# Performance work log

Measured on AMD Instinct MI355X. Metric: run time of the kernel, lower is better.

Reference implementation:

```python
import jax, jax.numpy as jnp
import numpy as np

THRESHOLD = 6.0  # bnb MatmulLtState outlier threshold


def setup_inputs() -> dict:
    key = jax.random.key(0)
    k1, k2, k3, k4, k5 = jax.random.split(key, 5)
    B, S, DIN, DOUT = 4, 2048, 4096, 16384
    x = jax.random.normal(k1, (B, S, DIN), dtype=jnp.float32).astype(jnp.float16)
    # inject a few outlier feature columns (|x| > threshold) so the LLM.int8()
    # mixed-precision decomposition path is actually exercised
    out_cols = jax.random.randint(k5, (8,), 0, DIN)
    x = x.at[:, :, out_cols].multiply(10.0)
    # CB: int8 codebook values stored as fp16 (bnb keeps them as int8; math is identical)
    CB = jnp.round(jax.random.uniform(k2, (DOUT, DIN), minval=-127.0, maxval=127.0)).astype(jnp.float16)
    SCB = jax.random.uniform(k3, (DOUT, 1), minval=0.5, maxval=2.0).astype(jnp.float16)
    bias = (jax.random.normal(k4, (DOUT,)) * 0.01).astype(jnp.float16)
    return {"x": x, "CB": CB, "SCB": SCB, "bias": bias}


def _llm_int8_matmul(x, CB, SCB, bias, threshold):
    # forward: weight = CB * SCB / 127 (dequantized fp16 weight), then bnb's
    # mixed int8 matmul with outlier-column decomposition (has_fp16_weights=True)
    W = CB.astype(jnp.float32) * SCB.astype(jnp.float32) / 127.0  # [DOUT, DIN]
    xf = x.astype(jnp.float32)
    lead = xf.shape[:-1]
    X = xf.reshape(-1, xf.shape[-1])  # [N, DIN]

    # outlier columns: any row has |x| > threshold in that feature column
    col_out = (jnp.abs(X) > threshold).any(axis=0)  # [DIN] bool
    X_out = jnp.where(col_out[None, :], X, 0.0)      # fp16-path activations
    X_in = jnp.where(col_out[None, :], 0.0, X)       # int8-path activations

    # per-row (per-token) absmax int8 quantization of inlier activations
    sx = jnp.maximum(jnp.max(jnp.abs(X_in), axis=1, keepdims=True), 1e-8)  # [N,1]
    Xq = jnp.clip(jnp.round(X_in * (127.0 / sx)), -127.0, 127.0)

    # per-output-row absmax int8 quantization of the (dequantized) weight
    sw = jnp.maximum(jnp.max(jnp.abs(W), axis=1, keepdims=True), 1e-8)  # [DOUT,1]
    Wq = jnp.clip(jnp.round(W * (127.0 / sw)), -127.0, 127.0)

    # int8 GEMM (emulated in fp32) + dequant with outer product of scales
    out = (Xq @ Wq.T) * (sx * sw.T) * (1.0 / (127.0 * 127.0))  # [N, DOUT]
    # fp16 outlier path: only the outlier weight columns participate
    out = out + X_out @ jnp.where(col_out[None, :], W, 0.0).T
    out = out + bias.astype(jnp.float32)[None, :]
    return out.reshape(*lead, W.shape[0]).astype(jnp.float16)


def reference(x, CB, SCB, bias):
    return _llm_int8_matmul(x, CB, SCB, bias, THRESHOLD)
```

## Files before the change

kernel.cpp:

```cpp
#include <hip/hip_runtime.h>
#include <hip/hip_fp16.h>
#include <stdint.h>

typedef int v4i __attribute__((ext_vector_type(4)));

__device__ __forceinline__ void gld_lds16(const void* g, void* l) {
    __builtin_amdgcn_global_load_lds(
        (const __attribute__((address_space(1))) void*)g,
        (__attribute__((address_space(3))) void*)l,
        16, 0, 0);
}

#define ENDBAR() do { __builtin_amdgcn_s_barrier(); __builtin_amdgcn_sched_barrier(0); } while (0)
#define VMC(n)   asm volatile("s_waitcnt vmcnt(" #n ")" ::: "memory")
#define VMLG0()  asm volatile("s_waitcnt vmcnt(0) lgkmcnt(0)" ::: "memory")

__global__ __launch_bounds__(256) void k_flags(const float* __restrict__ x,
                                               unsigned int* __restrict__ flags,
                                               int total4, int DIN) {
    int idx = blockIdx.x * blockDim.x + threadIdx.x;
    int stride = gridDim.x * blockDim.x;
    int dmask = DIN - 1;
    for (int i = idx; i < total4; i += stride) {
        float4 v = ((const float4*)x)[i];
        int base = i * 4;
        if (fabsf(v.x) > 6.0f) atomicOr(&flags[(base + 0) & dmask], 1u);
        if (fabsf(v.y) > 6.0f) atomicOr(&flags[(base + 1) & dmask], 1u);
        if (fabsf(v.z) > 6.0f) atomicOr(&flags[(base + 2) & dmask], 1u);
        if (fabsf(v.w) > 6.0f) atomicOr(&flags[(base + 3) & dmask], 1u);
    }
}

__global__ __launch_bounds__(256) void k_build(const unsigned int* __restrict__ flags,
                                               unsigned char* __restrict__ bmask,
                                               int* __restrict__ ncols,
                                               int* __restrict__ cols, int DIN) {
    __shared__ int wcnt[4];
    __shared__ int base;
    int tid = threadIdx.x, lane = tid & 63, wid = tid >> 6;
    if (tid == 0) base = 0;
    __syncthreads();
    for (int c0 = 0; c0 < DIN; c0 += 256) {
        int c = c0 + tid;
        bool p = (c < DIN) && (flags[c] != 0u);
        if (c < DIN) bmask[c] = p ? 1 : 0;
        unsigned long long m = __ballot(p);
        int wpre = __popcll(m & ((1ull << lane) - 1ull));
        if (lane == 0) wcnt[wid] = __popcll(m);
        __syncthreads();
        int pre = 0;
        for (int w = 0; w < wid; w++) pre += wcnt[w];
        if (p) cols[base + pre + wpre] = c;
        __syncthreads();
        if (tid == 0) base += wcnt[0] + wcnt[1] + wcnt[2] + wcnt[3];
        __syncthreads();
    }
    if (tid == 0) *ncols = base;
}

__global__ __launch_bounds__(256) void k_quantx(const float* __restrict__ x,
                                                const unsigned char* __restrict__ bmask,
                                                signed char* __restrict__ Xq,
                                                float* __restrict__ sx, int DIN) {
    int row = blockIdx.x;
    int tid = threadIdx.x, lane = tid & 63, wid = tid >> 6;
    const float* xr = x + (size_t)row * DIN;
    float f[16];
    #pragma unroll
    for (int j = 0; j < 4; j++) {
        float4 v = ((const float4*)xr)[tid * 4 + j];
        f[4*j] = v.x; f[4*j+1] = v.y; f[4*j+2] = v.z; f[4*j+3] = v.w;
    }
    uint4 bm4 = ((const uint4*)bmask)[tid];
    const unsigned char* bm = (const unsigned char*)&bm4;
    float m = 0.0f;
    #pragma unroll
    for (int j = 0; j < 16; j++) {
        if (bm[j]) f[j] = 0.0f;
        m = fmaxf(m, fabsf(f[j]));
    }
    #pragma unroll
    for (int off = 32; off >= 1; off >>= 1) m = fmaxf(m, __shfl_xor(m, off));
    __shared__ float red[4];
    if (lane == 0) red[wid] = m;
    __syncthreads();
    m = fmaxf(fmaxf(red[0], red[1]), fmaxf(red[2], red[3]));
    float sxv = fmaxf(m, 1e-8f);
    if (Xq) {
        float scale = 127.0f / sxv;
        int qi[16];
        #pragma unroll
        for (int j = 0; j < 16; j++) {
            float r = rintf(f[j] * scale);
            r = fminf(127.0f, fmaxf(-127.0f, r));
            qi[j] = (int)r;
        }
        int4 ov;
        ov.x = (qi[0]&0xff) | ((qi[1]&0xff)<<8) | ((qi[2]&0xff)<<16) | ((qi[3]&0xff)<<24);
        ov.y = (qi[4]&0xff) | ((qi[5]&0xff)<<8) | ((qi[6]&0xff)<<16) | ((qi[7]&0xff)<<24);
        ov.z = (qi[8]&0xff) | ((qi[9]&0xff)<<8) | ((qi[10]&0xff)<<16) | ((qi[11]&0xff)<<24);
        ov.w = (qi[12]&0xff) | ((qi[13]&0xff)<<8) | ((qi[14]&0xff)<<16) | ((qi[15]&0xff)<<24);
        ((int4*)(Xq + (size_t)row * DIN))[tid] = ov;
    }
    if (tid == 0) sx[row] = sxv;
}

__global__ __launch_bounds__(256) void k_quantw(const float* __restrict__ CB,
                                                const float* __restrict__ SCB,
                                                signed char* __restrict__ Wq,
                                                float* __restrict__ sw, int DIN) {
    int row = blockIdx.x;
    int tid = threadIdx.x, lane = tid & 63, wid = tid >> 6;
    float scb = SCB[row];
    const float* cr = CB + (size_t)row * DIN;
    float w[16];
    #pragma unroll
    for (int j = 0; j < 4; j++) {
        float4 v = ((const float4*)cr)[tid * 4 + j];
        w[4*j]   = v.x * scb / 127.0f;
        w[4*j+1] = v.y * scb / 127.0f;
        w[4*j+2] = v.z * scb / 127.0f;
        w[4*j+3] = v.w * scb / 127.0f;
    }
    float m = 0.0f;
    #pragma unroll
    for (int j = 0; j < 16; j++) m = fmaxf(m, fabsf(w[j]));
    #pragma unroll
    for (int off = 32; off >= 1; off >>= 1) m = fmaxf(m, __shfl_xor(m, off));
    __shared__ float red[4];
    if (lane == 0) red[wid] = m;
    __syncthreads();
    m = fmaxf(fmaxf(red[0], red[1]), fmaxf(red[2], red[3]));
    float swv = fmaxf(m, 1e-8f);
    if (Wq) {
        float scale = 127.0f / swv;
        int qi[16];
        #pragma unroll
        for (int j = 0; j < 16; j++) {
            float r = rintf(w[j] * scale);
            r = fminf(127.0f, fmaxf(-127.0f, r));
            qi[j] = (int)r;
        }
        int4 ov;
        ov.x = (qi[0]&0xff) | ((qi[1]&0xff)<<8) | ((qi[2]&0xff)<<16) | ((qi[3]&0xff)<<24);
        ov.y = (qi[4]&0xff) | ((qi[5]&0xff)<<8) | ((qi[6]&0xff)<<16) | ((qi[7]&0xff)<<24);
        ov.z = (qi[8]&0xff) | ((qi[9]&0xff)<<8) | ((qi[10]&0xff)<<16) | ((qi[11]&0xff)<<24);
        ov.w = (qi[12]&0xff) | ((qi[13]&0xff)<<8) | ((qi[14]&0xff)<<16) | ((qi[15]&0xff)<<24);
        ((int4*)(Wq + (size_t)row * DIN))[tid] = ov;
    }
    if (tid == 0) sw[row] = swv;
}

__global__ __launch_bounds__(256) void k_outpanels(
    const float* __restrict__ x, const float* __restrict__ CB,
    const float* __restrict__ SCB, const int* __restrict__ ncols,
    const int* __restrict__ cols, float* __restrict__ Xout, float* __restrict__ Wout,
    int Nrows, int DOUT, int DIN)
{
    int nc = *ncols;
    int ncl = nc < 16 ? nc : 16;
    int idx = blockIdx.x * 256 + threadIdx.x;
    int row = idx >> 4, c = idx & 15;
    if (row >= Nrows + DOUT) return;
    float v = 0.0f;
    if (row < Nrows) {
        if (c < ncl) v = x[(size_t)row * DIN + cols[c]];
        Xout[row * 16 + c] = v;
    } else {
        int j = row - Nrows;
        if (c < ncl) v = CB[(size_t)j * DIN + cols[c]] * SCB[j] / 127.0f;
        Wout[j * 16 + c] = v;
    }
}

__global__ __launch_bounds__(512) void k_gemm8(
    const signed char* __restrict__ Xq, const signed char* __restrict__ Wq,
    const float* __restrict__ sx, const float* __restrict__ sw,
    const float* __restrict__ x, const float* __restrict__ CB,
    const float* __restrict__ SCB, const float* __restrict__ bias,
    const float* __restrict__ Xout, const float* __restrict__ Wout,
    const int* __restrict__ ncols, const int* __restrict__ cols,
    float* __restrict__ out, int Nrows, int DOUT, int DIN)
{
    __shared__ __align__(16) char LDS[131072];

    const int tid = threadIdx.x, lane = tid & 63, wid = tid >> 6;
    const int wm = wid >> 2, wn = wid & 3;

    int nwg = gridDim.x, bid = blockIdx.x;
    int swzb;
    if ((nwg & 7) == 0) { int cpx = nwg >> 3; swzb = (bid & 7) * cpx + (bid >> 3); }
    else swzb = bid;
    int mtiles = Nrows >> 8;
    int ntiles = DOUT >> 8;
    int mt, ntl;
    if ((mtiles & 7) == 0 && (ntiles & 3) == 0 && (nwg & 31) == 0) {
        int group = swzb >> 5, local = swzb & 31;
        int mrects = mtiles >> 3;
        int mt_r = group % mrects, nt_r = group / mrects;
        mt  = (mt_r << 3) + (local & 7);
        ntl = (nt_r << 2) + (local >> 3);
    } else {
        mt = swzb % mtiles; ntl = swzb / mtiles;
    }
    int brow = mt << 8, bcol = ntl << 8;

    const int o0 = 16 * ((lane >> 4) ^ ((lane >> 1) & 7));
    const int o1 = o0 ^ 64;
    const int aRow = (wm * 128 + (lane & 15)) * 128;
    const int bRow = (wn * 64 + (lane & 15)) * 128;

    const int stRow = wid * 8 + (lane >> 3);
    const int stCol = 16 * ((lane & 7) ^ (((wid & 1) << 2) + (lane >> 4)));
    const signed char* aSrc = Xq + (size_t)(brow + stRow) * DIN + stCol;
    const signed char* bSrc = Wq + (size_t)(bcol + stRow) * DIN + stCol;
    const int ldsW = wid * 1024;

    v4i acc[8][4] = {};
    v4i a0[8], a1[8], b0[4], b1[4];

    const int nt = DIN >> 7;
    const int NIT = nt >> 1;

#define STAGE_HALF(srcBase, matOff, bf, h, kc)                                   \
    do { _Pragma("unroll")                                                        \
      for (int q = 0; q < 2; q++) {                                               \
        int seg = 2*(h) + q;                                                      \
        gld_lds16((srcBase) + (size_t)seg * 64 * DIN + (kc),                      \
                  &LDS[(matOff) + (bf)*32768 + seg*8192 + ldsW]);                 \
      }                                                                           \
    } while (0)

#define DS_A(dst, bf, miB)                                                        \
    do { _Pragma("unroll")                                                        \
      for (int mi = 0; mi < 4; mi++) {                                            \
        int ro = (bf)*32768 + aRow + ((miB) + mi) * 2048;                         \
        dst[mi*2+0] = *(const v4i*)&LDS[ro + o0];                                 \
        dst[mi*2+1] = *(const v4i*)&LDS[ro + o1];                                 \
      }                                                                           \
    } while (0)

#define DS_B(dst, bf, niB)                                                        \
    do { _Pragma("unroll")                                                        \
      for (int ni = 0; ni < 2; ni++) {                                            \
        int ro = 65536 + (bf)*32768 + bRow + ((niB) + ni) * 2048;                 \
        dst[ni*2+0] = *(const v4i*)&LDS[ro + o0];                                 \
        dst[ni*2+1] = *(const v4i*)&LDS[ro + o1];                                 \
      }                                                                           \
    } while (0)

#define QUAD(A8, B4, accM, accN)                                                  \
    do { __builtin_amdgcn_s_setprio(1); _Pragma("unroll")                         \
      for (int mi = 0; mi < 4; mi++) { _Pragma("unroll")                          \
        for (int ni = 0; ni < 2; ni++) { _Pragma("unroll")                        \
          for (int ks = 0; ks < 2; ks++)                                          \
            acc[(accM)+mi][(accN)+ni] = __builtin_amdgcn_mfma_i32_16x16x64_i8(    \
                A8[mi*2+ks], B4[ni*2+ks], acc[(accM)+mi][(accN)+ni], 0, 0, 0);    \
        } }                                                                       \
      __builtin_amdgcn_s_setprio(0);                                              \
    } while (0)

    STAGE_HALF(aSrc, 0,     0, 0, 0);
    STAGE_HALF(aSrc, 0,     0, 1, 0);
    STAGE_HALF(bSrc, 65536, 0, 0, 0);
    STAGE_HALF(bSrc, 65536, 0, 1, 0);
    STAGE_HALF(aSrc, 0,     1, 0, 128);
    STAGE_HALF(aSrc, 0,     1, 1, 128);
    VMC(4);
    ENDBAR();

    for (int it = 0; it < NIT; ++it) {
        int t = 2 * it;
        int kB1 = (t + 1) << 7;
        int tA2 = t + 2; if (tA2 > nt - 1) tA2 = nt - 1;
        int kA2 = tA2 << 7;
        int tA3 = t + 3; if (tA3 > nt - 1) tA3 = nt - 1;
        int kA3 = tA3 << 7;

        STAGE_HALF(bSrc, 65536, 1, 0, kB1);
        DS_B(b0, 0, 0); DS_A(a0, 0, 0);
        QUAD(a0, b0, 0, 0);
        STAGE_HALF(bSrc, 65536, 1, 1, kB1);
        DS_A(a1, 0, 4);
        QUAD(a1, b0, 4, 0);
        ENDBAR();
        STAGE_HALF(aSrc, 0, 0, 0, kA2);
        DS_B(b1, 0, 2);
        QUAD(a1, b1, 4, 2);
        STAGE_HALF(aSrc, 0, 0, 1, kA2);
        QUAD(a0, b1, 0, 2);
        VMC(4);
        ENDBAR();
        STAGE_HALF(bSrc, 65536, 0, 0, kA2);
        DS_B(b0, 1, 0); DS_A(a0, 1, 0);
        QUAD(a0, b0, 0, 0);
        STAGE_HALF(bSrc, 65536, 0, 1, kA2);
        DS_A(a1, 1, 4);
        QUAD(a1, b0, 4, 0);
        ENDBAR();
        STAGE_HALF(aSrc, 0, 1, 0, kA3);
        DS_B(b1, 1, 2);
        QUAD(a1, b1, 4, 2);
        STAGE_HALF(aSrc, 0, 1, 1, kA3);
        QUAD(a0, b1, 0, 2);
        VMC(4);
        ENDBAR();
    }
    VMLG0();
    ENDBAR();

    int nc = *ncols;
    int ncl = nc < 16 ? nc : 16;
    float* Xo = (float*)&LDS[0];
    float* Wo = (float*)&LDS[65536];
    for (int idx = tid; idx < 4096; idx += 512) {
        int i = idx >> 4, c = idx & 15;
        Xo[i * 17 + c] = Xout[(size_t)(brow + i) * 16 + c];
        Wo[i * 17 + c] = Wout[(size_t)(bcol + i) * 16 + c];
    }
    __syncthreads();

    float sww[4], bzz[4];
    #pragma unroll
    for (int ni = 0; ni < 4; ni++) {
        int gcol = bcol + wn * 64 + ni * 16 + (lane & 15);
        sww[ni] = sw[gcol];
        bzz[ni] = bias[gcol];
    }

    #pragma unroll
    for (int h = 0; h < 2; h++) {
        float vout[4][4][4];
        #pragma unroll
        for (int mi = 0; mi < 4; mi++) {
            int row = wm * 128 + (h * 4 + mi) * 16 + (lane >> 4) * 4;
            #pragma unroll
            for (int r = 0; r < 4; r++) {
                float sxv = sx[brow + row + r];
                #pragma unroll
                for (int ni = 0; ni < 4; ni++)
                    vout[mi][ni][r] =
                        ((float)acc[h * 4 + mi][ni][r] * (sxv * sww[ni])) * (1.0f / 16129.0f);
            }
        }
        for (int c = 0; c < ncl; c++) {
            float wo[4];
            #pragma unroll
            for (int ni = 0; ni < 4; ni++)
                wo[ni] = Wo[(wn * 64 + ni * 16 + (lane & 15)) * 17 + c];
            #pragma unroll
            for (int mi = 0; mi < 4; mi++) {
                int row = wm * 128 + (h * 4 + mi) * 16 + (lane >> 4) * 4;
                #pragma unroll
                for (int r = 0; r < 4; r++) {
                    float xo = Xo[(row + r) * 17 + c];
                    #pragma unroll
                    for (int ni = 0; ni < 4; ni++)
                        vout[mi][ni][r] += xo * wo[ni];
                }
            }
        }
        #pragma unroll
        for (int mi = 0; mi < 4; mi++) {
            #pragma unroll
            for (int ni = 0; ni < 4; ni++) {
                int gcol = bcol + wn * 64 + ni * 16 + (lane & 15);
                #pragma unroll
                for (int r = 0; r < 4; r++) {
                    int grow = brow + wm * 128 + (h * 4 + mi) * 16 + (lane >> 4) * 4 + r;
                    float v = vout[mi][ni][r];
                    for (int c = 16; c < nc; c++) {
                        int col = cols[c];
                        v += x[(size_t)grow * DIN + col] *
                             (CB[(size_t)gcol * DIN + col] * SCB[gcol] / 127.0f);
                    }
                    v += bzz[ni];
                    v = __half2float(__float2half(v));
                    out[(size_t)grow * DOUT + gcol] = v;
                }
            }
        }
    }
#undef STAGE_HALF
#undef DS_A
#undef DS_B
#undef QUAD
}

template<int FLY>
__global__ __launch_bounds__(256) void k_gemm(
    const signed char* __restrict__ Xq, const signed char* __restrict__ Wq,
    const float* __restrict__ sx, const float* __restrict__ sw,
    const float* __restrict__ x, const float* __restrict__ CB,
    const float* __restrict__ SCB, const float* __restrict__ bias,
    const unsigned char* __restrict__ bmask,
    const int* __restrict__ ncols, const int* __restrict__ cols,
    float* __restrict__ out, int Nrows, int DOUT, int DIN)
{
    __shared__ __align__(16) signed char Asm[128 * 64];
    __shared__ __align__(16) signed char Bsm[128 * 64];

    int nwg = gridDim.x;
    int bid = blockIdx.x;
    int swzb;
    if ((nwg & 7) == 0) { int cpx = nwg >> 3; swzb = (bid & 7) * cpx + (bid >> 3); }
    else swzb = bid;
    int mtiles = Nrows >> 7;
    int mt = swzb % mtiles;
    int nt = swzb / mtiles;
    int brow = mt << 7, bcol = nt << 7;

    int tid = threadIdx.x, lane = tid & 63, wid = tid >> 6;
    int wr = wid >> 1, wc = wid & 1;

    v4i acc[4][4] = {};

    int arow = wr * 64 + (lane & 15);
    int brl  = wc * 64 + (lane & 15);
    int kc   = (lane >> 4) * 16;

    if constexpr (FLY == 0) {
        int srow = lane >> 2;
        int scol = (lane & 3) * 16;
        const signed char* ga0 = Xq + (size_t)(brow + wid * 16 + srow) * DIN + scol;
        const signed char* ga1 = Xq + (size_t)(brow + (wid + 4) * 16 + srow) * DIN + scol;
        const signed char* gb0 = Wq + (size_t)(bcol + wid * 16 + srow) * DIN + scol;
        const signed char* gb1 = Wq + (size_t)(bcol + (wid + 4) * 16 + srow) * DIN + scol;
        signed char* la0 = &Asm[wid * 1024];
        signed char* la1 = &Asm[(wid + 4) * 1024];
        signed char* lb0 = &Bsm[wid * 1024];
        signed char* lb1 = &Bsm[(wid + 4) * 1024];

        for (int k0 = 0; k0 < DIN; k0 += 64) {
            gld_lds16(ga0 + k0, la0);
            gld_lds16(ga1 + k0, la1);
            gld_lds16(gb0 + k0, lb0);
            gld_lds16(gb1 + k0, lb1);
            __syncthreads();
            v4i a[4], b[4];
            #pragma unroll
            for (int mi = 0; mi < 4; mi++) a[mi] = *(const v4i*)&Asm[(arow + mi * 16) * 64 + kc];
            #pragma unroll
            for (int ni = 0; ni < 4; ni++) b[ni] = *(const v4i*)&Bsm[(brl + ni * 16) * 64 + kc];
            #pragma unroll
            for (int mi = 0; mi < 4; mi++)
                #pragma unroll
                for (int ni = 0; ni < 4; ni++)
                    acc[mi][ni] = __builtin_amdgcn_mfma_i32_16x16x64_i8(a[mi], b[ni], acc[mi][ni], 0, 0, 0);
            __syncthreads();
        }
    } else {
        int ra = tid >> 1, ca = (tid & 1) * 32;
        const float* xrow = x  + (size_t)(brow + ra) * DIN + ca;
        const float* crow = CB + (size_t)(bcol + ra) * DIN + ca;
        float xscale = 127.0f / sx[brow + ra];
        float scb    = SCB[bcol + ra];
        float wscale = 127.0f / sw[bcol + ra];
        signed char* lda = &Asm[ra * 64 + ca];
        signed char* ldb = &Bsm[ra * 64 + ca];

        for (int k0 = 0; k0 < DIN; k0 += 64) {
            float xa[32], wb[32];
            #pragma unroll
            for (int j = 0; j < 8; j++) {
                float4 v = ((const float4*)(xrow + k0))[j];
                xa[4*j] = v.x; xa[4*j+1] = v.y; xa[4*j+2] = v.z; xa[4*j+3] = v.w;
                float4 u = ((const float4*)(crow + k0))[j];
                wb[4*j] = u.x; wb[4*j+1] = u.y; wb[4*j+2] = u.z; wb[4*j+3] = u.w;
            }
            uint4 bm0 = *(const uint4*)(bmask + k0 + ca);
            uint4 bm1 = *(const uint4*)(bmask + k0 + ca + 16);
            const unsigned char* bmp0 = (const unsigned char*)&bm0;
            const unsigned char* bmp1 = (const unsigned char*)&bm1;
            int qa[32], qb[32];
            #pragma unroll
            for (int j = 0; j < 32; j++) {
                float fx = xa[j];
                if ((j < 16 ? bmp0[j] : bmp1[j - 16])) fx = 0.0f;
                float rx = rintf(fx * xscale);
                qa[j] = (int)fminf(127.0f, fmaxf(-127.0f, rx));
                float wv = wb[j] * scb / 127.0f;
                float rw = rintf(wv * wscale);
                qb[j] = (int)fminf(127.0f, fmaxf(-127.0f, rw));
            }
            int4 pa0, pa1, pb0, pb1;
            #pragma unroll
            for (int g = 0; g < 8; g++) {
                int vpk = (qa[4*g]&0xff) | ((qa[4*g+1]&0xff)<<8) | ((qa[4*g+2]&0xff)<<16) | ((qa[4*g+3]&0xff)<<24);
                if (g < 4) ((int*)&pa0)[g] = vpk; else ((int*)&pa1)[g-4] = vpk;
                int wpk = (qb[4*g]&0xff) | ((qb[4*g+1]&0xff)<<8) | ((qb[4*g+2]&0xff)<<16) | ((qb[4*g+3]&0xff)<<24);
                if (g < 4) ((int*)&pb0)[g] = wpk; else ((int*)&pb1)[g-4] = wpk;
            }
            __syncthreads();
            *(int4*)lda = pa0; *(int4*)(lda + 16) = pa1;
            *(int4*)ldb = pb0; *(int4*)(ldb + 16) = pb1;
            __syncthreads();
            v4i a[4], b[4];
            #pragma unroll
            for (int mi = 0; mi < 4; mi++) a[mi] = *(const v4i*)&Asm[(arow + mi * 16) * 64 + kc];
            #pragma unroll
            for (int ni = 0; ni < 4; ni++) b[ni] = *(const v4i*)&Bsm[(brl + ni * 16) * 64 + kc];
            #pragma unroll
            for (int mi = 0; mi < 4; mi++)
                #pragma unroll
                for (int ni = 0; ni < 4; ni++)
                    acc[mi][ni] = __builtin_amdgcn_mfma_i32_16x16x64_i8(a[mi], b[ni], acc[mi][ni], 0, 0, 0);
        }
        __syncthreads();
    }

    int nc = *ncols;
    int ncl = nc < 16 ? nc : 16;
    float* Xo = (float*)Asm;
    float* Wo = (float*)Bsm;
    for (int idx = tid; idx < 2048; idx += 256) {
        int i = idx >> 4, c = idx & 15;
        if (c < ncl) {
            int col = cols[c];
            Xo[idx] = x[(size_t)(brow + i) * DIN + col];
            Wo[idx] = CB[(size_t)(bcol + i) * DIN + col] * SCB[bcol + i] / 127.0f;
        }
    }
    __syncthreads();

    #pragma unroll
    for (int mi = 0; mi < 4; mi++) {
        #pragma unroll
        for (int ni = 0; ni < 4; ni++) {
            int rl0 = wr * 64 + mi * 16 + (lane >> 4) * 4;
            int cl  = wc * 64 + ni * 16 + (lane & 15);
            int gcol = bcol + cl;
            float swv = sw[gcol];
            float bz = bias[gcol];
            #pragma unroll
            for (int r = 0; r < 4; r++) {
                int grow = brow + rl0 + r;
                float v = ((float)acc[mi][ni][r] * (sx[grow] * swv)) * (1.0f / 16129.0f);
                float osum = 0.0f;
                for (int c = 0; c < ncl; c++)
                    osum += Xo[(rl0 + r) * 16 + c] * Wo[cl * 16 + c];
                for (int c = 16; c < nc; c++) {
                    int col = cols[c];
                    osum += x[(size_t)grow * DIN + col] *
                            (CB[(size_t)gcol * DIN + col] * SCB[gcol] / 127.0f);
                }
                v = v + osum;
                v = v + bz;
                v = __half2float(__float2half(v));
                out[(size_t)grow * DOUT + gcol] = v;
            }
        }
    }
}

static constexpr size_t FLAGS_OFF = 0;
static constexpr size_t BMASK_OFF = 16384;
static constexpr size_t NCOLS_OFF = 20480;
static constexpr size_t COLS_OFF  = 20544;
static constexpr size_t SX_OFF    = 36992;
static constexpr size_t SW_OFF    = 69760;
static constexpr size_t DYN_OFF   = 262144;

extern "C" void kernel_launch(void* const* d_in, const int* in_sizes, int n_in,
                              void* d_out, int out_size, void* d_ws, size_t ws_size,
                              hipStream_t stream) {
    const float* x    = (const float*)d_in[0];
    const float* CB   = (const float*)d_in[1];
    const float* SCB  = (const float*)d_in[2];
    const float* bias = (const float*)d_in[3];

    int DOUT  = in_sizes[2];
    int DIN   = in_sizes[1] / DOUT;
    int Nrows = in_sizes[0] / DIN;

    char* ws = (char*)d_ws;
    unsigned int* flags = (unsigned int*)(ws + FLAGS_OFF);
    unsigned char* bmask = (unsigned char*)(ws + BMASK_OFF);
    int* ncols = (int*)(ws + NCOLS_OFF);
    int* cols  = (int*)(ws + COLS_OFF);
    float* sx  = (float*)(ws + SX_OFF);
    float* sw  = (float*)(ws + SW_OFF);

    size_t off = DYN_OFF;
    float* Xout = (float*)(ws + off); off += (size_t)Nrows * 16 * 4;
    float* Wout = (float*)(ws + off); off += (size_t)DOUT * 16 * 4;
    signed char* Xq = (signed char*)(ws + off); off += (size_t)Nrows * DIN;
    signed char* Wq = (signed char*)(ws + off); off += (size_t)DOUT * DIN;
    size_t need = off;
    float* out = (float*)d_out;

    bool bigws = ws_size >= need;
    bool can8  = bigws && (Nrows % 256 == 0) && (DOUT % 256 == 0) && (DIN % 256 == 0);

    hipMemsetAsync(ws + FLAGS_OFF, 0, 16384, stream);
    k_flags<<<2048, 256, 0, stream>>>(x, flags, Nrows * DIN / 4, DIN);
    k_build<<<1, 256, 0, stream>>>(flags, bmask, ncols, cols, DIN);
    k_quantx<<<Nrows, 256, 0, stream>>>(x, bmask, bigws ? Xq : nullptr, sx, DIN);
    k_quantw<<<DOUT, 256, 0, stream>>>(CB, SCB, bigws ? Wq : nullptr, sw, DIN);

    if (can8) {
        int total_threads = (Nrows + DOUT) * 16;
        int nblk = (total_threads + 255) / 256;
        k_outpanels<<<nblk, 256, 0, stream>>>(
            x, CB, SCB, ncols, cols, Xout, Wout, Nrows, DOUT, DIN);
        int ngrid = (Nrows / 256) * (DOUT / 256);
        k_gemm8<<<ngrid, 512, 0, stream>>>(Xq, Wq, sx, sw, x, CB, SCB, bias,
                                           Xout, Wout, ncols, cols, out, Nrows, DOUT, DIN);
    } else if (bigws) {
        int ngrid = (Nrows / 128) * (DOUT / 128);
        k_gemm<0><<<ngrid, 256, 0, stream>>>(Xq, Wq, sx, sw, x, CB, SCB, bias,
                                             bmask, ncols, cols, out, Nrows, DOUT, DIN);
    } else {
        int ngrid = (Nrows / 128) * (DOUT / 128);
        k_gemm<1><<<ngrid, 256, 0, stream>>>(nullptr, nullptr, sx, sw, x, CB, SCB, bias,
                                             bmask, ncols, cols, out, Nrows, DOUT, DIN);
    }
}
```

Before: 692.9 us.

## Switch int8 GEMM to 32x32x32 MFMA and fold outlier panels into quant kernels

```diff
diff --git a/kernel.cpp b/kernel.cpp
--- a/kernel.cpp
+++ b/kernel.cpp
@@ -2,7 +2,8 @@
 #include <hip/hip_fp16.h>
 #include <stdint.h>
 
-typedef int v4i __attribute__((ext_vector_type(4)));
+typedef int v4i  __attribute__((ext_vector_type(4)));
+typedef int v16i __attribute__((ext_vector_type(16)));
 
 __device__ __forceinline__ void gld_lds16(const void* g, void* l) {
     __builtin_amdgcn_global_load_lds(
@@ -61,7 +62,10 @@
 __global__ __launch_bounds__(256) void k_quantx(const float* __restrict__ x,
                                                 const unsigned char* __restrict__ bmask,
                                                 signed char* __restrict__ Xq,
-                                                float* __restrict__ sx, int DIN) {
+                                                float* __restrict__ sx,
+                                                float* __restrict__ Xout,
+                                                const int* __restrict__ ncols,
+                                                const int* __restrict__ cols, int DIN) {
     int row = blockIdx.x;
     int tid = threadIdx.x, lane = tid & 63, wid = tid >> 6;
     const float* xr = x + (size_t)row * DIN;
@@ -102,13 +106,23 @@
         ov.w = (qi[12]&0xff) | ((qi[13]&0xff)<<8) | ((qi[14]&0xff)<<16) | ((qi[15]&0xff)<<24);
         ((int4*)(Xq + (size_t)row * DIN))[tid] = ov;
     }
+    if (tid < 16) {
+        int nc = *ncols;
+        int ncl = nc < 16 ? nc : 16;
+        float v = 0.0f;
+        if (tid < ncl) v = xr[cols[tid]];
+        Xout[(size_t)row * 16 + tid] = v;
+    }
     if (tid == 0) sx[row] = sxv;
 }
 
 __global__ __launch_bounds__(256) void k_quantw(const float* __restrict__ CB,
                                                 const float* __restrict__ SCB,
                                                 signed char* __restrict__ Wq,
-                                                float* __restrict__ sw, int DIN) {
+                                                float* __restrict__ sw,
+                                                float* __restrict__ Wout,
+                                                const int* __restrict__ ncols,
+                                                const int* __restrict__ cols, int DIN) {
     int row = blockIdx.x;
     int tid = threadIdx.x, lane = tid & 63, wid = tid >> 6;
     float scb = SCB[row];
@@ -148,32 +162,17 @@
         ov.w = (qi[12]&0xff) | ((qi[13]&0xff)<<8) | ((qi[14]&0xff)<<16) | ((qi[15]&0xff)<<24);
         ((int4*)(Wq + (size_t)row * DIN))[tid] = ov;
     }
+    if (tid < 16) {
+        int nc = *ncols;
+        int ncl = nc < 16 ? nc : 16;
+        float v = 0.0f;
+        if (tid < ncl) v = cr[cols[tid]] * scb / 127.0f;
+        Wout[(size_t)row * 16 + tid] = v;
+    }
     if (tid == 0) sw[row] = swv;
 }
 
-__global__ __launch_bounds__(256) void k_outpanels(
-    const float* __restrict__ x, const float* __restrict__ CB,
-    const float* __restrict__ SCB, const int* __restrict__ ncols,
-    const int* __restrict__ cols, float* __restrict__ Xout, float* __restrict__ Wout,
-    int Nrows, int DOUT, int DIN)
-{
-    int nc = *ncols;
-    int ncl = nc < 16 ? nc : 16;
-    int idx = blockIdx.x * 256 + threadIdx.x;
-    int row = idx >> 4, c = idx & 15;
-    if (row >= Nrows + DOUT) return;
-    float v = 0.0f;
-    if (row < Nrows) {
-        if (c < ncl) v = x[(size_t)row * DIN + cols[c]];
-        Xout[row * 16 + c] = v;
-    } else {
-        int j = row - Nrows;
-        if (c < ncl) v = CB[(size_t)j * DIN + cols[c]] * SCB[j] / 127.0f;
-        Wout[j * 16 + c] = v;
-    }
-}
-
-__global__ __launch_bounds__(512) void k_gemm8(
+__global__ __launch_bounds__(512) void k_gemm32(
     const signed char* __restrict__ Xq, const signed char* __restrict__ Wq,
     const float* __restrict__ sx, const float* __restrict__ sw,
     const float* __restrict__ x, const float* __restrict__ CB,
@@ -186,6 +185,7 @@
 
     const int tid = threadIdx.x, lane = tid & 63, wid = tid >> 6;
     const int wm = wid >> 2, wn = wid & 3;
+    const int hi = lane >> 5;
 
     int nwg = gridDim.x, bid = blockIdx.x;
     int swzb;
@@ -200,15 +200,18 @@
         int mt_r = group % mrects, nt_r = group / mrects;
         mt  = (mt_r << 3) + (local & 7);
         ntl = (nt_r << 2) + (local >> 3);
-    } else {
-        mt = swzb % mtiles; ntl = swzb / mtiles;
-    }
+    } else { mt = swzb % mtiles; ntl = swzb / mtiles; }
     int brow = mt << 8, bcol = ntl << 8;
 
-    const int o0 = 16 * ((lane >> 4) ^ ((lane >> 1) & 7));
-    const int o1 = o0 ^ 64;
-    const int aRow = (wm * 128 + (lane & 15)) * 128;
-    const int bRow = (wn * 64 + (lane & 15)) * 128;
+    const int sw7 = (lane >> 1) & 7;
+    int o[4];
+    #pragma unroll
+    for (int ks = 0; ks < 4; ks++) o[ks] = 16 * (((ks << 1) | hi) ^ sw7);
+    int aR[4], bR[2];
+    #pragma unroll
+    for (int mi = 0; mi < 4; mi++) aR[mi] = (wm * 128 + mi * 32 + (lane & 31)) * 128;
+    #pragma unroll
+    for (int ni = 0; ni < 2; ni++) bR[ni] = 65536 + (wn * 64 + ni * 32 + (lane & 31)) * 128;
 
     const int stRow = wid * 8 + (lane >> 3);
     const int stCol = 16 * ((lane & 7) ^ (((wid & 1) << 2) + (lane >> 4)));
@@ -216,8 +219,8 @@
     const signed char* bSrc = Wq + (size_t)(bcol + stRow) * DIN + stCol;
     const int ldsW = wid * 1024;
 
-    v4i acc[8][4] = {};
-    v4i a0[8], a1[8], b0[4], b1[4];
+    v16i acc[4][2] = {};
+    v4i aF[16], bW[4];
 
     const int nt = DIN >> 7;
     const int NIT = nt >> 1;
@@ -231,31 +234,29 @@
       }                                                                           \
     } while (0)
 
-#define DS_A(dst, bf, miB)                                                        \
+#define READ_A(bf)                                                                \
     do { _Pragma("unroll")                                                        \
-      for (int mi = 0; mi < 4; mi++) {                                            \
-        int ro = (bf)*32768 + aRow + ((miB) + mi) * 2048;                         \
-        dst[mi*2+0] = *(const v4i*)&LDS[ro + o0];                                 \
-        dst[mi*2+1] = *(const v4i*)&LDS[ro + o1];                                 \
+      for (int mi = 0; mi < 4; mi++) { _Pragma("unroll")                          \
+        for (int ks = 0; ks < 4; ks++)                                            \
+          aF[mi*4+ks] = *(const v4i*)&LDS[(bf)*32768 + aR[mi] + o[ks]];           \
       }                                                                           \
     } while (0)
 
-#define DS_B(dst, bf, niB)                                                        \
+#define READ_B(bf, ksB)                                                           \
     do { _Pragma("unroll")                                                        \
-      for (int ni = 0; ni < 2; ni++) {                                            \
-        int ro = 65536 + (bf)*32768 + bRow + ((niB) + ni) * 2048;                 \
-        dst[ni*2+0] = *(const v4i*)&LDS[ro + o0];                                 \
-        dst[ni*2+1] = *(const v4i*)&LDS[ro + o1];                                 \
+      for (int ni = 0; ni < 2; ni++) { _Pragma("unroll")                          \
+        for (int dk = 0; dk < 2; dk++)                                            \
+          bW[ni*2+dk] = *(const v4i*)&LDS[(bf)*32768 + bR[ni] + o[(ksB)+dk]];     \
       }                                                                           \
     } while (0)
 
-#define QUAD(A8, B4, accM, accN)                                                  \
+#define MFMA16(ksB)                                                               \
     do { __builtin_amdgcn_s_setprio(1); _Pragma("unroll")                         \
       for (int mi = 0; mi < 4; mi++) { _Pragma("unroll")                          \
         for (int ni = 0; ni < 2; ni++) { _Pragma("unroll")                        \
-          for (int ks = 0; ks < 2; ks++)                                          \
-            acc[(accM)+mi][(accN)+ni] = __builtin_amdgcn_mfma_i32_16x16x64_i8(    \
-                A8[mi*2+ks], B4[ni*2+ks], acc[(accM)+mi][(accN)+ni], 0, 0, 0);    \
+          for (int dk = 0; dk < 2; dk++)                                          \
+            acc[mi][ni] = __builtin_amdgcn_mfma_i32_32x32x32_i8(                  \
+                aF[mi*4+(ksB)+dk], bW[ni*2+dk], acc[mi][ni], 0, 0, 0);            \
         } }                                                                       \
       __builtin_amdgcn_s_setprio(0);                                              \
     } while (0)
@@ -278,31 +279,25 @@
         int kA3 = tA3 << 7;
 
         STAGE_HALF(bSrc, 65536, 1, 0, kB1);
-        DS_B(b0, 0, 0); DS_A(a0, 0, 0);
-        QUAD(a0, b0, 0, 0);
+        READ_A(0); READ_B(0, 0);
+        MFMA16(0);
         STAGE_HALF(bSrc, 65536, 1, 1, kB1);
-        DS_A(a1, 0, 4);
-        QUAD(a1, b0, 4, 0);
         ENDBAR();
         STAGE_HALF(aSrc, 0, 0, 0, kA2);
-        DS_B(b1, 0, 2);
-        QUAD(a1, b1, 4, 2);
+        READ_B(0, 2);
+        MFMA16(2);
         STAGE_HALF(aSrc, 0, 0, 1, kA2);
-        QUAD(a0, b1, 0, 2);
         VMC(4);
         ENDBAR();
         STAGE_HALF(bSrc, 65536, 0, 0, kA2);
-        DS_B(b0, 1, 0); DS_A(a0, 1, 0);
-        QUAD(a0, b0, 0, 0);
+        READ_A(1); READ_B(1, 0);
+        MFMA16(0);
         STAGE_HALF(bSrc, 65536, 0, 1, kA2);
-        DS_A(a1, 1, 4);
-        QUAD(a1, b0, 4, 0);
         ENDBAR();
         STAGE_HALF(aSrc, 0, 1, 0, kA3);
-        DS_B(b1, 1, 2);
-        QUAD(a1, b1, 4, 2);
+        READ_B(1, 2);
+        MFMA16(2);
         STAGE_HALF(aSrc, 0, 1, 1, kA3);
-        QUAD(a0, b1, 0, 2);
         VMC(4);
         ENDBAR();
     }
@@ -320,71 +315,62 @@
     }
     __syncthreads();
 
-    float sww[4], bzz[4];
-    #pragma unroll
-    for (int ni = 0; ni < 4; ni++) {
-        int gcol = bcol + wn * 64 + ni * 16 + (lane & 15);
+    float sww[2], bzz[2];
+    #pragma unroll
+    for (int ni = 0; ni < 2; ni++) {
+        int gcol = bcol + wn * 64 + ni * 32 + (lane & 31);
         sww[ni] = sw[gcol];
         bzz[ni] = bias[gcol];
     }
 
     #pragma unroll
-    for (int h = 0; h < 2; h++) {
-        float vout[4][4][4];
+    for (int mi = 0; mi < 4; mi++) {
+        float sxr[16];
         #pragma unroll
-        for (int mi = 0; mi < 4; mi++) {
-            int row = wm * 128 + (h * 4 + mi) * 16 + (lane >> 4) * 4;
-            #pragma unroll
-            for (int r = 0; r < 4; r++) {
-                float sxv = sx[brow + row + r];
-                #pragma unroll
-                for (int ni = 0; ni < 4; ni++)
-                    vout[mi][ni][r] =
-                        ((float)acc[h * 4 + mi][ni][r] * (sxv * sww[ni])) * (1.0f / 16129.0f);
+        for (int rg = 0; rg < 16; rg++) {
+            int rowD = (rg & 3) + 8 * (rg >> 2) + 4 * hi;
+            sxr[rg] = sx[brow + wm * 128 + mi * 32 + rowD];
+        }
+        float vout[2][16];
+        #pragma unroll
+        for (int ni = 0; ni < 2; ni++)
+            #pragma unroll
+            for (int rg = 0; rg < 16; rg++)
+                vout[ni][rg] = ((float)acc[mi][ni][rg] * (sxr[rg] * sww[ni])) * (1.0f / 16129.0f);
+        for (int c = 0; c < ncl; c++) {
+            float wo0 = Wo[(wn * 64 + (lane & 31)) * 17 + c];
+            float wo1 = Wo[(wn * 64 + 32 + (lane & 31)) * 17 + c];
+            #pragma unroll
+            for (int rg = 0; rg < 16; rg++) {
+                int rowD = (rg & 3) + 8 * (rg >> 2) + 4 * hi;
+                float xo = Xo[(wm * 128 + mi * 32 + rowD) * 17 + c];
+                vout[0][rg] += xo * wo0;
+                vout[1][rg] += xo * wo1;
             }
         }
-        for (int c = 0; c < ncl; c++) {
-            float wo[4];
-            #pragma unroll
-            for (int ni = 0; ni < 4; ni++)
-                wo[ni] = Wo[(wn * 64 + ni * 16 + (lane & 15)) * 17 + c];
-            #pragma unroll
-            for (int mi = 0; mi < 4; mi++) {
-                int row = wm * 128 + (h * 4 + mi) * 16 + (lane >> 4) * 4;
-                #pragma unroll
-                for (int r = 0; r < 4; r++) {
-                    float xo = Xo[(row + r) * 17 + c];
-                    #pragma unroll
-                    for (int ni = 0; ni < 4; ni++)
-                        vout[mi][ni][r] += xo * wo[ni];
+        #pragma unroll
+        for (int ni = 0; ni < 2; ni++) {
+            int gcol = bcol + wn * 64 + ni * 32 + (lane & 31);
+            #pragma unroll
+            for (int rg = 0; rg < 16; rg++) {
+                int rowD = (rg & 3) + 8 * (rg >> 2) + 4 * hi;
+                int grow = brow + wm * 128 + mi * 32 + rowD;
+                float v = vout[ni][rg];
+                for (int c2 = 16; c2 < nc; c2++) {
+                    int col = cols[c2];
+                    v += x[(size_t)grow * DIN + col] *
+                         (CB[(size_t)gcol * DIN + col] * SCB[gcol] / 127.0f);
                 }
+                v += bzz[ni];
+                v = __half2float(__float2half(v));
+                out[(size_t)grow * DOUT + gcol] = v;
             }
         }
-        #pragma unroll
-        for (int mi = 0; mi < 4; mi++) {
-            #pragma unroll
-            for (int ni = 0; ni < 4; ni++) {
-                int gcol = bcol + wn * 64 + ni * 16 + (lane & 15);
-                #pragma unroll
-                for (int r = 0; r < 4; r++) {
-                    int grow = brow + wm * 128 + (h * 4 + mi) * 16 + (lane >> 4) * 4 + r;
-                    float v = vout[mi][ni][r];
-                    for (int c = 16; c < nc; c++) {
-                        int col = cols[c];
-                        v += x[(size_t)grow * DIN + col] *
-                             (CB[(size_t)gcol * DIN + col] * SCB[gcol] / 127.0f);
-                    }
-                    v += bzz[ni];
-                    v = __half2float(__float2half(v));
-                    out[(size_t)grow * DOUT + gcol] = v;
-                }
-            }
-        }
     }
 #undef STAGE_HALF
-#undef DS_A
-#undef DS_B
-#undef QUAD
+#undef READ_A
+#undef READ_B
+#undef MFMA16
 }
 
 template<int FLY>
@@ -595,18 +581,16 @@
     hipMemsetAsync(ws + FLAGS_OFF, 0, 16384, stream);
     k_flags<<<2048, 256, 0, stream>>>(x, flags, Nrows * DIN / 4, DIN);
     k_build<<<1, 256, 0, stream>>>(flags, bmask, ncols, cols, DIN);
-    k_quantx<<<Nrows, 256, 0, stream>>>(x, bmask, bigws ? Xq : nullptr, sx, DIN);
-    k_quantw<<<DOUT, 256, 0, stream>>>(CB, SCB, bigws ? Wq : nullptr, sw, DIN);
+    k_quantx<<<Nrows, 256, 0, stream>>>(x, bmask, bigws ? Xq : nullptr, sx,
+                                        Xout, ncols, cols, DIN);
+    k_quantw<<<DOUT, 256, 0, stream>>>(CB, SCB, bigws ? Wq : nullptr, sw,
+                                       Wout, ncols, cols, DIN);
 
     if (can8) {
-        int total_threads = (Nrows + DOUT) * 16;
-        int nblk = (total_threads + 255) / 256;
-        k_outpanels<<<nblk, 256, 0, stream>>>(
-            x, CB, SCB, ncols, cols, Xout, Wout, Nrows, DOUT, DIN);
         int ngrid = (Nrows / 256) * (DOUT / 256);
-        k_gemm8<<<ngrid, 512, 0, stream>>>(Xq, Wq, sx, sw, x, CB, SCB, bias,
-                                           Xout, Wout, ncols, cols, out, Nrows, DOUT, DIN);
-    } else if (bigws) {
+        k_gemm32<<<ngrid, 512, 0, stream>>>(Xq, Wq, sx, sw, x, CB, SCB, bias,
+                                            Xout, Wout, ncols, cols, out, Nrows, DOUT, DIN);
+    } else if (bigws && (Nrows % 128 == 0) && (DOUT % 128 == 0) && (DIN % 64 == 0)) {
         int ngrid = (Nrows / 128) * (DOUT / 128);
         k_gemm<0><<<ngrid, 256, 0, stream>>>(Xq, Wq, sx, sw, x, CB, SCB, bias,
                                              bmask, ncols, cols, out, Nrows, DOUT, DIN);
```

Result: slower. 774.7 us (+11.8%).
